# Kernel optimization log

Hardware: AMD Instinct MI355X
Metric: run time of the kernel (lower is better)

The kernel has to match this reference:

```python
import jax, jax.numpy as jnp
import numpy as np

INPUT_SIZE = 1024
HIDDEN_SIZE = 1024
BATCH = 8192
MLP_H1, MLP_H2 = 16, 8


def _uniform(key, shape, stdv):
    return jax.random.uniform(key, shape, jnp.float32, -stdv, stdv)


def setup_inputs() -> dict:
    key = jax.random.key(0)
    ks = jax.random.split(key, 20)
    stdv = 1.0 / np.sqrt(HIDDEN_SIZE)
    I, H = INPUT_SIZE, HIDDEN_SIZE
    inp = {
        "x": jax.random.normal(ks[0], (BATCH, I), jnp.float32),
        "h": jax.random.normal(ks[1], (BATCH, H), jnp.float32),
        "c": jax.random.normal(ks[2], (BATCH, H), jnp.float32),
        # gate weights (torch layout: matmul(h, W_h*) + matmul(x, W_x*) + b)
        "W_hi": _uniform(ks[3], (H, H), stdv),
        "W_xi": _uniform(ks[4], (I, H), stdv),
        "b_i": _uniform(ks[5], (H,), stdv),
        "W_hc": _uniform(ks[6], (H, H), stdv),
        "W_xc": _uniform(ks[7], (I, H), stdv),
        "b_c": _uniform(ks[8], (H,), stdv),
        "W_ho": _uniform(ks[9], (H, H), stdv),
        "W_xo": _uniform(ks[10], (I, H), stdv),
        "b_o": _uniform(ks[11], (H,), stdv),
        # forget MLP: (I+H) -> 16 -> 8 -> H, ReLU hidden, sigmoid output
        "W1": _uniform(ks[12], (I + H, MLP_H1), stdv),
        "b1": _uniform(ks[13], (MLP_H1,), stdv),
        "W2": _uniform(ks[14], (MLP_H1, MLP_H2), stdv),
        "b2": _uniform(ks[15], (MLP_H2,), stdv),
        "W3": _uniform(ks[16], (MLP_H2, H), stdv),
        "b3": _uniform(ks[17], (H,), stdv),
    }
    return inp


def reference(x, h, c, W_hi, W_xi, b_i, W_hc, W_xc, b_c, W_ho, W_xo, b_o,
              W1, b1, W2, b2, W3, b3):
    # forget gate via small MLP on concat(x, h)
    xh = jnp.concatenate((x, h), axis=1)           # [B, I+H]
    z = jax.nn.relu(xh @ W1 + b1)                  # [B, 16]
    z = jax.nn.relu(z @ W2 + b2)                   # [B, 8]
    f = jax.nn.sigmoid(z @ W3 + b3)                # [B, H]

    i = jax.nn.sigmoid(h @ W_hi + x @ W_xi + b_i)
    g = jnp.tanh(h @ W_hc + x @ W_xc + b_c)
    o = jax.nn.sigmoid(h @ W_ho + x @ W_xo + b_o)

    c_new = f * c + i * g
    h_new = o * jnp.tanh(c_new)
    return (h_new, c_new, f)
```

## Files before the change

### kernel.cpp

```cpp
#include <hip/hip_runtime.h>
#include <math.h>

#define BATCH 8192
#define HDIM  1024
#define KDIM  2048
#define NDIM  3072

typedef __attribute__((ext_vector_type(8))) short short8;
typedef __attribute__((ext_vector_type(4))) float floatx4;

__device__ __forceinline__ float b2f(unsigned short u) {
  union { unsigned int i; float f; } v; v.i = ((unsigned int)u) << 16; return v.f;
}
__device__ __forceinline__ unsigned short f2b(float f) {
  union { unsigned int i; float f; } v; v.f = f;
  unsigned int r = v.i + 0x7FFFu + ((v.i >> 16) & 1u);
  return (unsigned short)(r >> 16);
}
__device__ __forceinline__ float ldsel(const void* p, size_t i, int isbf) {
  return isbf ? b2f(((const unsigned short*)p)[i]) : ((const float*)p)[i];
}
__device__ __forceinline__ float sigf(float x) { return 1.0f / (1.0f + __expf(-x)); }
__device__ __forceinline__ float tanhfast(float x) {
  float a = __builtin_fabsf(x);
  float t = __expf(-2.f * a);
  float r = (1.f - t) / (1.f + t);
  return copysignf(r, x);
}

__device__ __forceinline__ int detect_bf(const void* x) {
  unsigned int w = ((const unsigned int*)x)[threadIdx.x & 63];
  unsigned short lo = (unsigned short)(w & 0xFFFFu);
  int e = (lo >> 7) & 0xFF;
  bool ok = (e >= 110 && e <= 135) || ((lo & 0x7FFFu) == 0);
  unsigned long long m = __ballot(ok);
  return (__popcll(m) >= 48) ? 1 : 0;
}

__device__ __forceinline__ void gld16(const void* g, void* l) {
  auto gp = reinterpret_cast<__attribute__((address_space(1))) unsigned int*>(
      (unsigned long long)g);
  auto lp = reinterpret_cast<__attribute__((address_space(3))) unsigned int*>(
      (unsigned long long)l);
  __builtin_amdgcn_global_load_lds(gp, lp, 16, 0, 0);
}

__device__ __forceinline__ short8 ld8bf(const void* p, size_t off, int isbf) {
  short8 r;
  if (isbf) {
    r = *(const short8*)((const unsigned short*)p + off);
  } else {
    const float* s = (const float*)p + off;
    float4 a = *(const float4*)(s);
    float4 b = *(const float4*)(s + 4);
    r[0]=(short)f2b(a.x); r[1]=(short)f2b(a.y); r[2]=(short)f2b(a.z); r[3]=(short)f2b(a.w);
    r[4]=(short)f2b(b.x); r[5]=(short)f2b(b.y); r[6]=(short)f2b(b.z); r[7]=(short)f2b(b.w);
  }
  return r;
}

__global__ __launch_bounds__(256) void k_z2(
    const void* __restrict__ x, const void* __restrict__ h,
    const void* __restrict__ W1, const void* __restrict__ b1,
    const void* __restrict__ W2, const void* __restrict__ b2,
    float* __restrict__ z2) {
  __shared__ __align__(16) char smem[70976];
  const int isbf = detect_bf(x);
  const int tid = threadIdx.x;
  unsigned short* lW = (unsigned short*)smem;
  float* part = (float*)(smem + 65536);
  float* z1s  = (float*)(smem + 69888);
  const int m0 = blockIdx.x * 16;
#pragma unroll
  for (int it = 0; it < 16; ++it) {
    const int chunk = it * 256 + tid;
    const int k = chunk >> 1;
    const int jh = (chunk & 1) * 8;
    unsigned short v[8];
    if (isbf) {
      short8 s = *(const short8*)((const unsigned short*)W1 + (size_t)k * 16 + jh);
#pragma unroll
      for (int j = 0; j < 8; ++j) v[j] = (unsigned short)s[j];
    } else {
      const float* s = (const float*)W1 + (size_t)k * 16 + jh;
      float4 a = *(const float4*)(s);
      float4 b = *(const float4*)(s + 4);
      v[0]=f2b(a.x); v[1]=f2b(a.y); v[2]=f2b(a.z); v[3]=f2b(a.w);
      v[4]=f2b(b.x); v[5]=f2b(b.y); v[6]=f2b(b.z); v[7]=f2b(b.w);
    }
#pragma unroll
    for (int j = 0; j < 8; ++j) {
      const int row = jh + j;
      lW[row * 2048 + (((k >> 3) ^ (row & 7)) << 3) + (k & 7)] = v[j];
    }
  }
  __syncthreads();
  const int w = tid >> 6;
  const int lane = tid & 63;
  const int q = lane >> 4;
  const int r = lane & 15;
  const void* src = (w >> 1) ? h : x;
  const size_t abase = (size_t)(m0 + r) * 1024 + (w & 1) * 512;
  const int kb = (w >> 1) * 1024 + (w & 1) * 512;
  floatx4 acc = {0.f, 0.f, 0.f, 0.f};
#pragma unroll 4
  for (int kt = 0; kt < 16; ++kt) {
    const int kl = kt * 32 + q * 8;
    short8 a = ld8bf(src, abase + kl, isbf);
    const int kg = kb + kl;
    short8 b = *(const short8*)(lW + r * 2048 + (((kg >> 3) ^ (r & 7)) << 3));
    acc = __builtin_amdgcn_mfma_f32_16x16x32_bf16(a, b, acc, 0, 0, 0);
  }
#pragma unroll
  for (int t = 0; t < 4; ++t) part[(w * 16 + q * 4 + t) * 17 + r] = acc[t];
  __syncthreads();
  {
    const int row = tid >> 4;
    const int n = tid & 15;
    float s = part[(0 * 16 + row) * 17 + n] + part[(1 * 16 + row) * 17 + n] +
              part[(2 * 16 + row) * 17 + n] + part[(3 * 16 + row) * 17 + n] +
              ldsel(b1, (size_t)n, isbf);
    z1s[row * 17 + n] = fmaxf(s, 0.f);
  }
  __syncthreads();
  if (tid < 128) {
    const int row = tid >> 3;
    const int p = tid & 7;
    float s = ldsel(b2, (size_t)p, isbf);
#pragma unroll
    for (int nn = 0; nn < 16; ++nn)
      s += z1s[row * 17 + nn] * ldsel(W2, (size_t)nn * 8 + p, isbf);
    z2[(size_t)(m0 + row) * 8 + p] = fmaxf(s, 0.f);
  }
}

__global__ __launch_bounds__(256) void k_wt(
    const void* __restrict__ x,
    const void* __restrict__ wxi, const void* __restrict__ whi,
    const void* __restrict__ wxc, const void* __restrict__ whc,
    const void* __restrict__ wxo, const void* __restrict__ who,
    unsigned short* __restrict__ WT) {
  __shared__ __align__(16) float tbuf[64][65];
  const int isbf = detect_bf(x);
  const int tid = threadIdx.x;
  const int b = blockIdx.x;
  const int mat = b >> 8;
  const int rem = b & 255;
  const int ti = rem >> 4;
  const int tj = rem & 15;
  const void* Ws[6] = {wxi, whi, wxc, whc, wxo, who};
  const void* W = Ws[mat];
  const int gt = mat >> 1;
  const int half = mat & 1;
  const int rrow = tid >> 3;
  const int c8 = (tid & 7) * 8;
#pragma unroll
  for (int it = 0; it < 2; ++it) {
    int row = it * 32 + rrow;
    size_t off = (size_t)(ti * 64 + row) * 1024 + tj * 64 + c8;
    if (isbf) {
      const unsigned short* s = (const unsigned short*)W + off;
      ushort4 a = *(const ushort4*)(s);
      ushort4 bv = *(const ushort4*)(s + 4);
      tbuf[row][c8+0]=b2f(a.x);  tbuf[row][c8+1]=b2f(a.y);
      tbuf[row][c8+2]=b2f(a.z);  tbuf[row][c8+3]=b2f(a.w);
      tbuf[row][c8+4]=b2f(bv.x); tbuf[row][c8+5]=b2f(bv.y);
      tbuf[row][c8+6]=b2f(bv.z); tbuf[row][c8+7]=b2f(bv.w);
    } else {
      const float* s = (const float*)W + off;
      float4 a = *(const float4*)(s);
      float4 bv = *(const float4*)(s + 4);
      tbuf[row][c8+0]=a.x;  tbuf[row][c8+1]=a.y;  tbuf[row][c8+2]=a.z;  tbuf[row][c8+3]=a.w;
      tbuf[row][c8+4]=bv.x; tbuf[row][c8+5]=bv.y; tbuf[row][c8+6]=bv.z; tbuf[row][c8+7]=bv.w;
    }
  }
  __syncthreads();
#pragma unroll
  for (int it = 0; it < 2; ++it) {
    int nl = it * 32 + rrow;
    int n = gt * 1024 + tj * 64 + nl;
    int kk = half * 1024 + ti * 64 + c8;
    short8 pk;
#pragma unroll
    for (int i = 0; i < 8; ++i) pk[i] = (short)f2b(tbuf[c8 + i][nl]);
    *(short8*)(WT + (size_t)n * KDIM + kk) = pk;
  }
}

__global__ __launch_bounds__(256) void k_apack(
    const void* __restrict__ x, const void* __restrict__ h,
    unsigned short* __restrict__ A) {
  if (detect_bf(x)) return;
  const size_t t0 = (size_t)blockIdx.x * 256 + threadIdx.x;
#pragma unroll
  for (int it = 0; it < 4; ++it) {
    const size_t idx = (t0 + (size_t)it * 524288) * 8;
    const int k = (int)(idx & 2047);
    const size_t m = idx >> 11;
    const float* s = (k < 1024) ? (const float*)x + m * 1024 + k
                                : (const float*)h + m * 1024 + (k - 1024);
    float4 a = *(const float4*)(s);
    float4 b = *(const float4*)(s + 4);
    short8 pk;
    pk[0]=(short)f2b(a.x); pk[1]=(short)f2b(a.y); pk[2]=(short)f2b(a.z); pk[3]=(short)f2b(a.w);
    pk[4]=(short)f2b(b.x); pk[5]=(short)f2b(b.y); pk[6]=(short)f2b(b.z); pk[7]=(short)f2b(b.w);
    *(short8*)(A + idx) = pk;
  }
}

__global__ __launch_bounds__(256, 3) void k_gemm(
    const void* __restrict__ x, const void* __restrict__ h,
    const unsigned short* __restrict__ Apack,
    const unsigned short* __restrict__ WT,
    unsigned short* __restrict__ P) {
  const int isbf = detect_bf(x);
  const unsigned short* Ax = isbf ? (const unsigned short*)x : Apack;
  const unsigned short* Ah = isbf ? (const unsigned short*)h : (Apack + 1024);
  const int sA = isbf ? 1024 : 2048;
  __shared__ __align__(16) unsigned short lA[128 * 64];
  __shared__ __align__(16) unsigned short lB[128 * 64];
  const int tid = threadIdx.x;
  const int lane = tid & 63;
  const int wv = tid >> 6;
  const int wm = (wv >> 1) << 6;
  const int wn = (wv & 1) << 6;
  const int m0 = blockIdx.y << 7;
  const int n0 = blockIdx.x << 7;

  floatx4 acc[4][4];
  const floatx4 fzero = {0.f, 0.f, 0.f, 0.f};
#pragma unroll
  for (int i = 0; i < 4; ++i)
#pragma unroll
    for (int j = 0; j < 4; ++j) acc[i][j] = fzero;

  int rr[4], kk[4];
#pragma unroll
  for (int ps = 0; ps < 4; ++ps) {
    int chunk = ps * 256 + tid;
    rr[ps] = chunk >> 3;
    kk[ps] = (chunk & 7) ^ (rr[ps] & 7);
  }
  const int px0 = (lane >> 4) ^ (lane & 7);
  const int px1 = ((lane >> 4) + 4) ^ (lane & 7);
  const int rowA = wm + (lane & 15);
  const int rowB = wn + (lane & 15);

  for (int kt = 0; kt < KDIM / 64; ++kt) {
    const int k0 = kt * 64;
    const unsigned short* Abase = (k0 < 1024) ? (Ax + k0) : (Ah + (k0 - 1024));
#pragma unroll
    for (int ps = 0; ps < 4; ++ps) {
      const int chunk = ps * 256 + tid;
      gld16(Abase + (size_t)(m0 + rr[ps]) * sA + kk[ps] * 8, lA + chunk * 8);
      gld16(WT + ((size_t)(n0 + rr[ps]) * KDIM + k0 + kk[ps] * 8), lB + chunk * 8);
    }
    __syncthreads();
#pragma unroll
    for (int s = 0; s < 2; ++s) {
      const int px = s ? px1 : px0;
      short8 af[4], bfr[4];
#pragma unroll
      for (int i = 0; i < 4; ++i)
        af[i] = *(const short8*)(lA + ((((rowA + (i << 4)) << 3) + px) << 3));
#pragma unroll
      for (int i = 0; i < 4; ++i)
        bfr[i] = *(const short8*)(lB + ((((rowB + (i << 4)) << 3) + px) << 3));
#pragma unroll
      for (int mi = 0; mi < 4; ++mi)
#pragma unroll
        for (int ni = 0; ni < 4; ++ni)
          acc[mi][ni] = __builtin_amdgcn_mfma_f32_16x16x32_bf16(
              af[mi], bfr[ni], acc[mi][ni], 0, 0, 0);
    }
    __syncthreads();
  }
  const int col = lane & 15;
  const int rq = (lane >> 4) << 2;
#pragma unroll
  for (int mi = 0; mi < 4; ++mi) {
#pragma unroll
    for (int ni = 0; ni < 4; ++ni) {
      const size_t n = (size_t)(n0 + wn + (ni << 4) + col);
#pragma unroll
      for (int t = 0; t < 4; ++t) {
        const size_t m = (size_t)(m0 + wm + (mi << 4) + rq + t);
        P[m * NDIM + n] = f2b(acc[mi][ni][t]);
      }
    }
  }
}

__global__ __launch_bounds__(256) void k_pointwise(
    const unsigned short* __restrict__ P, const void* __restrict__ x,
    const void* __restrict__ cin,
    const void* __restrict__ bi, const void* __restrict__ bc,
    const void* __restrict__ bo, const float* __restrict__ z2,
    const void* __restrict__ W3, const void* __restrict__ b3,
    void* __restrict__ out) {
  const int isbf = detect_bf(x);
  const int tid = threadIdx.x;
  const int n = tid * 4;
  const size_t MH = (size_t)BATCH * HDIM;

  float w3r[8][4], bif[4], bcf[4], bof[4], b3f[4];
  if (isbf) {
#pragma unroll
    for (int j = 0; j < 8; ++j) {
      ushort4 u = *(const ushort4*)((const unsigned short*)W3 + j * 1024 + n);
      w3r[j][0]=b2f(u.x); w3r[j][1]=b2f(u.y); w3r[j][2]=b2f(u.z); w3r[j][3]=b2f(u.w);
    }
    ushort4 u3 = *(const ushort4*)((const unsigned short*)b3 + n);
    b3f[0]=b2f(u3.x); b3f[1]=b2f(u3.y); b3f[2]=b2f(u3.z); b3f[3]=b2f(u3.w);
    ushort4 a = *(const ushort4*)((const unsigned short*)bi + n);
    ushort4 b = *(const ushort4*)((const unsigned short*)bc + n);
    ushort4 d = *(const ushort4*)((const unsigned short*)bo + n);
    bif[0]=b2f(a.x); bif[1]=b2f(a.y); bif[2]=b2f(a.z); bif[3]=b2f(a.w);
    bcf[0]=b2f(b.x); bcf[1]=b2f(b.y); bcf[2]=b2f(b.z); bcf[3]=b2f(b.w);
    bof[0]=b2f(d.x); bof[1]=b2f(d.y); bof[2]=b2f(d.z); bof[3]=b2f(d.w);
  } else {
#pragma unroll
    for (int j = 0; j < 8; ++j) {
      float4 u = *(const float4*)((const float*)W3 + j * 1024 + n);
      w3r[j][0]=u.x; w3r[j][1]=u.y; w3r[j][2]=u.z; w3r[j][3]=u.w;
    }
    float4 u3 = *(const float4*)((const float*)b3 + n);
    b3f[0]=u3.x; b3f[1]=u3.y; b3f[2]=u3.z; b3f[3]=u3.w;
    float4 a = *(const float4*)((const float*)bi + n);
    float4 b = *(const float4*)((const float*)bc + n);
    float4 d = *(const float4*)((const float*)bo + n);
    bif[0]=a.x; bif[1]=a.y; bif[2]=a.z; bif[3]=a.w;
    bcf[0]=b.x; bcf[1]=b.y; bcf[2]=b.z; bcf[3]=b.w;
    bof[0]=d.x; bof[1]=d.y; bof[2]=d.z; bof[3]=d.w;
  }

  const size_t m0 = (size_t)blockIdx.x * 8;
#pragma unroll
  for (int rI = 0; rI < 8; ++rI) {
    const size_t m = m0 + rI;
    const size_t idx = m * 1024 + n;
    const unsigned short* pr = P + m * NDIM + n;
    ushort4 ui = *(const ushort4*)(pr);
    ushort4 ug = *(const ushort4*)(pr + 1024);
    ushort4 uo = *(const ushort4*)(pr + 2048);
    float pi[4] = {b2f(ui.x), b2f(ui.y), b2f(ui.z), b2f(ui.w)};
    float pg[4] = {b2f(ug.x), b2f(ug.y), b2f(ug.z), b2f(ug.w)};
    float po[4] = {b2f(uo.x), b2f(uo.y), b2f(uo.z), b2f(uo.w)};
    float4 za = *(const float4*)(z2 + m * 8);
    float4 zb = *(const float4*)(z2 + m * 8 + 4);
    float zz[8] = {za.x, za.y, za.z, za.w, zb.x, zb.y, zb.z, zb.w};
    float cf[4];
    if (isbf) {
      ushort4 e = *(const ushort4*)((const unsigned short*)cin + idx);
      cf[0]=b2f(e.x); cf[1]=b2f(e.y); cf[2]=b2f(e.z); cf[3]=b2f(e.w);
    } else {
      float4 e = *(const float4*)((const float*)cin + idx);
      cf[0]=e.x; cf[1]=e.y; cf[2]=e.z; cf[3]=e.w;
    }
    float f3[4] = {b3f[0], b3f[1], b3f[2], b3f[3]};
#pragma unroll
    for (int j = 0; j < 8; ++j) {
      f3[0] += zz[j] * w3r[j][0];
      f3[1] += zz[j] * w3r[j][1];
      f3[2] += zz[j] * w3r[j][2];
      f3[3] += zz[j] * w3r[j][3];
    }
    float hn[4], cn[4], ff[4];
#pragma unroll
    for (int t = 0; t < 4; ++t) {
      float F = sigf(f3[t]);
      float I = sigf(pi[t] + bif[t]);
      float G = tanhfast(pg[t] + bcf[t]);
      float O = sigf(po[t] + bof[t]);
      float C = F * cf[t] + I * G;
      ff[t] = F;
      cn[t] = C;
      hn[t] = O * tanhfast(C);
    }
    if (isbf) {
      unsigned short* ob = (unsigned short*)out;
      *(ushort4*)(ob + idx) = make_ushort4(f2b(hn[0]), f2b(hn[1]), f2b(hn[2]), f2b(hn[3]));
      *(ushort4*)(ob + MH + idx) = make_ushort4(f2b(cn[0]), f2b(cn[1]), f2b(cn[2]), f2b(cn[3]));
      *(ushort4*)(ob + 2 * MH + idx) = make_ushort4(f2b(ff[0]), f2b(ff[1]), f2b(ff[2]), f2b(ff[3]));
    } else {
      float* ob = (float*)out;
      *(float4*)(ob + idx) = make_float4(hn[0], hn[1], hn[2], hn[3]);
      *(float4*)(ob + MH + idx) = make_float4(cn[0], cn[1], cn[2], cn[3]);
      *(float4*)(ob + 2 * MH + idx) = make_float4(ff[0], ff[1], ff[2], ff[3]);
    }
  }
}

extern "C" void kernel_launch(void* const* d_in, const int* in_sizes, int n_in,
                              void* d_out, int out_size, void* d_ws, size_t ws_size,
                              hipStream_t stream) {
  const void* x    = d_in[0];
  const void* h    = d_in[1];
  const void* c    = d_in[2];
  const void* W_hi = d_in[3];
  const void* W_xi = d_in[4];
  const void* b_i  = d_in[5];
  const void* W_hc = d_in[6];
  const void* W_xc = d_in[7];
  const void* b_c  = d_in[8];
  const void* W_ho = d_in[9];
  const void* W_xo = d_in[10];
  const void* b_o  = d_in[11];
  const void* W1   = d_in[12];
  const void* b1   = d_in[13];
  const void* W2   = d_in[14];
  const void* b2   = d_in[15];
  const void* W3   = d_in[16];
  const void* b3   = d_in[17];

  char* ws = (char*)d_ws;
  unsigned short* A   = (unsigned short*)ws;
  unsigned short* WT  = (unsigned short*)(ws + 33554432);
  unsigned short* P   = (unsigned short*)(ws + 46137344);
  float*          z2b = (float*)(ws + 96468992);

  k_apack<<<dim3(2048), dim3(256), 0, stream>>>(x, h, A);
  k_wt<<<dim3(1536), dim3(256), 0, stream>>>(x, W_xi, W_hi, W_xc, W_hc,
                                             W_xo, W_ho, WT);
  k_z2<<<dim3(512), dim3(256), 0, stream>>>(x, h, W1, b1, W2, b2, z2b);
  k_gemm<<<dim3(NDIM / 128, BATCH / 128), dim3(256), 0, stream>>>(x, h, A, WT, P);
  k_pointwise<<<dim3(BATCH / 8), dim3(256), 0, stream>>>(P, x, c, b_i, b_c, b_o,
                                                         z2b, W3, b3, d_out);
}
```

Before: 364.9 us.

## Fuse gate GEMM with LSTM pointwise epilogue and fold A packing into MLP kernel

The k_apack kernel goes away, and the k_z2 kernel now writes the bf16-packed x|h matrix as a side effect of reading it for the forget MLP. The GEMM is restructured so each block computes a 128x64 tile for all three gates at once, with three accumulator groups. The full LSTM pointwise math runs in the GEMM epilogue, which removes the intermediate P buffer round trip and the separate pointwise kernel. A grouped block-index swizzle is added for L2 reuse. The cost is higher register pressure (96 accumulators per thread, and occupancy hint dropped), plus epilogue stores that are scalar and strided rather than vectorized.

```diff
diff --git a/kernel.cpp b/kernel.cpp
--- a/kernel.cpp
+++ b/kernel.cpp
@@ -4,7 +4,6 @@
 #define BATCH 8192
 #define HDIM  1024
 #define KDIM  2048
-#define NDIM  3072
 
 typedef __attribute__((ext_vector_type(8))) short short8;
 typedef __attribute__((ext_vector_type(4))) float floatx4;
@@ -63,7 +62,7 @@
     const void* __restrict__ x, const void* __restrict__ h,
     const void* __restrict__ W1, const void* __restrict__ b1,
     const void* __restrict__ W2, const void* __restrict__ b2,
-    float* __restrict__ z2) {
+    unsigned short* __restrict__ A, float* __restrict__ z2) {
   __shared__ __align__(16) char smem[70976];
   const int isbf = detect_bf(x);
   const int tid = threadIdx.x;
@@ -108,6 +107,7 @@
     const int kl = kt * 32 + q * 8;
     short8 a = ld8bf(src, abase + kl, isbf);
     const int kg = kb + kl;
+    if (!isbf) *(short8*)(A + (size_t)(m0 + r) * KDIM + kg) = a;
     short8 b = *(const short8*)(lW + r * 2048 + (((kg >> 3) ^ (r & 7)) << 3));
     acc = __builtin_amdgcn_mfma_f32_16x16x32_bf16(a, b, acc, 0, 0, 0);
   }
@@ -187,59 +187,58 @@
   }
 }
 
-__global__ __launch_bounds__(256) void k_apack(
-    const void* __restrict__ x, const void* __restrict__ h,
-    unsigned short* __restrict__ A) {
-  if (detect_bf(x)) return;
-  const size_t t0 = (size_t)blockIdx.x * 256 + threadIdx.x;
-#pragma unroll
-  for (int it = 0; it < 4; ++it) {
-    const size_t idx = (t0 + (size_t)it * 524288) * 8;
-    const int k = (int)(idx & 2047);
-    const size_t m = idx >> 11;
-    const float* s = (k < 1024) ? (const float*)x + m * 1024 + k
-                                : (const float*)h + m * 1024 + (k - 1024);
-    float4 a = *(const float4*)(s);
-    float4 b = *(const float4*)(s + 4);
-    short8 pk;
-    pk[0]=(short)f2b(a.x); pk[1]=(short)f2b(a.y); pk[2]=(short)f2b(a.z); pk[3]=(short)f2b(a.w);
-    pk[4]=(short)f2b(b.x); pk[5]=(short)f2b(b.y); pk[6]=(short)f2b(b.z); pk[7]=(short)f2b(b.w);
-    *(short8*)(A + idx) = pk;
-  }
-}
-
-__global__ __launch_bounds__(256, 3) void k_gemm(
+__global__ __launch_bounds__(256) void k_gemm_f(
     const void* __restrict__ x, const void* __restrict__ h,
     const unsigned short* __restrict__ Apack,
     const unsigned short* __restrict__ WT,
-    unsigned short* __restrict__ P) {
+    const void* __restrict__ cin,
+    const void* __restrict__ bi, const void* __restrict__ bc,
+    const void* __restrict__ bo,
+    const float* __restrict__ z2,
+    const void* __restrict__ W3, const void* __restrict__ b3,
+    void* __restrict__ out) {
   const int isbf = detect_bf(x);
   const unsigned short* Ax = isbf ? (const unsigned short*)x : Apack;
   const unsigned short* Ah = isbf ? (const unsigned short*)h : (Apack + 1024);
-  const int sA = isbf ? 1024 : 2048;
-  __shared__ __align__(16) unsigned short lA[128 * 64];
-  __shared__ __align__(16) unsigned short lB[128 * 64];
+  const int sA = isbf ? 1024 : KDIM;
+  __shared__ __align__(16) char smem[40960];
+  unsigned short* lA = (unsigned short*)smem;
+  unsigned short* lB = (unsigned short*)(smem + 16384);
   const int tid = threadIdx.x;
   const int lane = tid & 63;
   const int wv = tid >> 6;
   const int wm = (wv >> 1) << 6;
-  const int wn = (wv & 1) << 6;
-  const int m0 = blockIdx.y << 7;
-  const int n0 = blockIdx.x << 7;
-
-  floatx4 acc[4][4];
+  const int wn = (wv & 1) << 5;
+
+  const int bid = blockIdx.x;
+  const int swz = ((bid & 7) << 7) | (bid >> 3);
+  const int m0 = (swz >> 4) << 7;
+  const int n0 = (swz & 15) << 6;
+
+  floatx4 acc[3][4][2];
   const floatx4 fzero = {0.f, 0.f, 0.f, 0.f};
 #pragma unroll
-  for (int i = 0; i < 4; ++i)
-#pragma unroll
-    for (int j = 0; j < 4; ++j) acc[i][j] = fzero;
-
-  int rr[4], kk[4];
+  for (int g = 0; g < 3; ++g)
+#pragma unroll
+    for (int i = 0; i < 4; ++i)
+#pragma unroll
+      for (int j = 0; j < 2; ++j) acc[g][i][j] = fzero;
+
+  int rrA[4], kkA[4];
 #pragma unroll
   for (int ps = 0; ps < 4; ++ps) {
-    int chunk = ps * 256 + tid;
-    rr[ps] = chunk >> 3;
-    kk[ps] = (chunk & 7) ^ (rr[ps] & 7);
+    int c = ps * 256 + tid;
+    rrA[ps] = c >> 3;
+    kkA[ps] = (c & 7) ^ (rrA[ps] & 7);
+  }
+  int gB[6], rrB[6], kkB[6];
+#pragma unroll
+  for (int ps = 0; ps < 6; ++ps) {
+    int c = ps * 256 + tid;
+    gB[ps] = c >> 9;
+    int cl = c & 511;
+    rrB[ps] = cl >> 3;
+    kkB[ps] = (cl & 7) ^ (rrB[ps] & 7);
   }
   const int px0 = (lane >> 4) ^ (lane & 7);
   const int px1 = ((lane >> 4) + 4) ^ (lane & 7);
@@ -251,142 +250,95 @@
     const unsigned short* Abase = (k0 < 1024) ? (Ax + k0) : (Ah + (k0 - 1024));
 #pragma unroll
     for (int ps = 0; ps < 4; ++ps) {
-      const int chunk = ps * 256 + tid;
-      gld16(Abase + (size_t)(m0 + rr[ps]) * sA + kk[ps] * 8, lA + chunk * 8);
-      gld16(WT + ((size_t)(n0 + rr[ps]) * KDIM + k0 + kk[ps] * 8), lB + chunk * 8);
+      const int c = ps * 256 + tid;
+      gld16(Abase + (size_t)(m0 + rrA[ps]) * sA + kkA[ps] * 8, lA + c * 8);
+    }
+#pragma unroll
+    for (int ps = 0; ps < 6; ++ps) {
+      const int c = ps * 256 + tid;
+      gld16(WT + ((size_t)(gB[ps] * 1024 + n0 + rrB[ps]) * KDIM + k0 + kkB[ps] * 8),
+            lB + c * 8);
     }
     __syncthreads();
 #pragma unroll
     for (int s = 0; s < 2; ++s) {
       const int px = s ? px1 : px0;
-      short8 af[4], bfr[4];
+      short8 af[4], bfr[3][2];
 #pragma unroll
       for (int i = 0; i < 4; ++i)
         af[i] = *(const short8*)(lA + ((((rowA + (i << 4)) << 3) + px) << 3));
 #pragma unroll
-      for (int i = 0; i < 4; ++i)
-        bfr[i] = *(const short8*)(lB + ((((rowB + (i << 4)) << 3) + px) << 3));
-#pragma unroll
-      for (int mi = 0; mi < 4; ++mi)
-#pragma unroll
-        for (int ni = 0; ni < 4; ++ni)
-          acc[mi][ni] = __builtin_amdgcn_mfma_f32_16x16x32_bf16(
-              af[mi], bfr[ni], acc[mi][ni], 0, 0, 0);
+      for (int g = 0; g < 3; ++g)
+#pragma unroll
+        for (int j = 0; j < 2; ++j)
+          bfr[g][j] = *(const short8*)(lB + (g << 12) +
+                                       ((((rowB + (j << 4)) << 3) + px) << 3));
+#pragma unroll
+      for (int g = 0; g < 3; ++g)
+#pragma unroll
+        for (int mi = 0; mi < 4; ++mi)
+#pragma unroll
+          for (int ni = 0; ni < 2; ++ni)
+            acc[g][mi][ni] = __builtin_amdgcn_mfma_f32_16x16x32_bf16(
+                af[mi], bfr[g][ni], acc[g][mi][ni], 0, 0, 0);
     }
     __syncthreads();
   }
-  const int col = lane & 15;
+
+  float* z2s = (float*)smem;
+  *(float4*)(z2s + tid * 4) = *(const float4*)(z2 + (size_t)m0 * 8 + tid * 4);
+  __syncthreads();
+
+  const int col_l = lane & 15;
   const int rq = (lane >> 4) << 2;
+  float w3c[2][8], b3c[2], bic[2], bcc[2], boc[2];
+#pragma unroll
+  for (int ni = 0; ni < 2; ++ni) {
+    const size_t n_g = (size_t)(n0 + wn + (ni << 4) + col_l);
+    b3c[ni] = ldsel(b3, n_g, isbf);
+    bic[ni] = ldsel(bi, n_g, isbf);
+    bcc[ni] = ldsel(bc, n_g, isbf);
+    boc[ni] = ldsel(bo, n_g, isbf);
+#pragma unroll
+    for (int j = 0; j < 8; ++j) w3c[ni][j] = ldsel(W3, (size_t)j * 1024 + n_g, isbf);
+  }
+  const size_t MH = (size_t)BATCH * HDIM;
 #pragma unroll
   for (int mi = 0; mi < 4; ++mi) {
 #pragma unroll
-    for (int ni = 0; ni < 4; ++ni) {
-      const size_t n = (size_t)(n0 + wn + (ni << 4) + col);
-#pragma unroll
-      for (int t = 0; t < 4; ++t) {
-        const size_t m = (size_t)(m0 + wm + (mi << 4) + rq + t);
-        P[m * NDIM + n] = f2b(acc[mi][ni][t]);
+    for (int t = 0; t < 4; ++t) {
+      const int rloc = wm + (mi << 4) + rq + t;
+      const size_t m_g = (size_t)m0 + rloc;
+      float zz[8];
+#pragma unroll
+      for (int j = 0; j < 8; ++j) zz[j] = z2s[rloc * 8 + j];
+#pragma unroll
+      for (int ni = 0; ni < 2; ++ni) {
+        const size_t n_g = (size_t)(n0 + wn + (ni << 4) + col_l);
+        const size_t idx = m_g * HDIM + n_g;
+        float f3 = b3c[ni];
+#pragma unroll
+        for (int j = 0; j < 8; ++j) f3 += zz[j] * w3c[ni][j];
+        const float cf = isbf ? b2f(((const unsigned short*)cin)[idx])
+                              : ((const float*)cin)[idx];
+        const float F = sigf(f3);
+        const float I = sigf(acc[0][mi][ni][t] + bic[ni]);
+        const float G = tanhfast(acc[1][mi][ni][t] + bcc[ni]);
+        const float O = sigf(acc[2][mi][ni][t] + boc[ni]);
+        const float C = F * cf + I * G;
+        const float HN = O * tanhfast(C);
+        if (isbf) {
+          unsigned short* ob = (unsigned short*)out;
+          ob[idx] = f2b(HN);
+          ob[MH + idx] = f2b(C);
+          ob[2 * MH + idx] = f2b(F);
+        } else {
+          float* ob = (float*)out;
+          ob[idx] = HN;
+          ob[MH + idx] = C;
+          ob[2 * MH + idx] = F;
+        }
       }
-    }
-  }
-}
-
-__global__ __launch_bounds__(256) void k_pointwise(
-    const unsigned short* __restrict__ P, const void* __restrict__ x,
-    const void* __restrict__ cin,
-    const void* __restrict__ bi, const void* __restrict__ bc,
-    const void* __restrict__ bo, const float* __restrict__ z2,
-    const void* __restrict__ W3, const void* __restrict__ b3,
-    void* __restrict__ out) {
-  const int isbf = detect_bf(x);
-  const int tid = threadIdx.x;
-  const int n = tid * 4;
-  const size_t MH = (size_t)BATCH * HDIM;
-
-  float w3r[8][4], bif[4], bcf[4], bof[4], b3f[4];
-  if (isbf) {
-#pragma unroll
-    for (int j = 0; j < 8; ++j) {
-      ushort4 u = *(const ushort4*)((const unsigned short*)W3 + j * 1024 + n);
-      w3r[j][0]=b2f(u.x); w3r[j][1]=b2f(u.y); w3r[j][2]=b2f(u.z); w3r[j][3]=b2f(u.w);
-    }
-    ushort4 u3 = *(const ushort4*)((const unsigned short*)b3 + n);
-    b3f[0]=b2f(u3.x); b3f[1]=b2f(u3.y); b3f[2]=b2f(u3.z); b3f[3]=b2f(u3.w);
-    ushort4 a = *(const ushort4*)((const unsigned short*)bi + n);
-    ushort4 b = *(const ushort4*)((const unsigned short*)bc + n);
-    ushort4 d = *(const ushort4*)((const unsigned short*)bo + n);
-    bif[0]=b2f(a.x); bif[1]=b2f(a.y); bif[2]=b2f(a.z); bif[3]=b2f(a.w);
-    bcf[0]=b2f(b.x); bcf[1]=b2f(b.y); bcf[2]=b2f(b.z); bcf[3]=b2f(b.w);
-    bof[0]=b2f(d.x); bof[1]=b2f(d.y); bof[2]=b2f(d.z); bof[3]=b2f(d.w);
-  } else {
-#pragma unroll
-    for (int j = 0; j < 8; ++j) {
-      float4 u = *(const float4*)((const float*)W3 + j * 1024 + n);
-      w3r[j][0]=u.x; w3r[j][1]=u.y; w3r[j][2]=u.z; w3r[j][3]=u.w;
-    }
-    float4 u3 = *(const float4*)((const float*)b3 + n);
-    b3f[0]=u3.x; b3f[1]=u3.y; b3f[2]=u3.z; b3f[3]=u3.w;
-    float4 a = *(const float4*)((const float*)bi + n);
-    float4 b = *(const float4*)((const float*)bc + n);
-    float4 d = *(const float4*)((const float*)bo + n);
-    bif[0]=a.x; bif[1]=a.y; bif[2]=a.z; bif[3]=a.w;
-    bcf[0]=b.x; bcf[1]=b.y; bcf[2]=b.z; bcf[3]=b.w;
-    bof[0]=d.x; bof[1]=d.y; bof[2]=d.z; bof[3]=d.w;
-  }
-
-  const size_t m0 = (size_t)blockIdx.x * 8;
-#pragma unroll
-  for (int rI = 0; rI < 8; ++rI) {
-    const size_t m = m0 + rI;
-    const size_t idx = m * 1024 + n;
-    const unsigned short* pr = P + m * NDIM + n;
-    ushort4 ui = *(const ushort4*)(pr);
-    ushort4 ug = *(const ushort4*)(pr + 1024);
-    ushort4 uo = *(const ushort4*)(pr + 2048);
-    float pi[4] = {b2f(ui.x), b2f(ui.y), b2f(ui.z), b2f(ui.w)};
-    float pg[4] = {b2f(ug.x), b2f(ug.y), b2f(ug.z), b2f(ug.w)};
-    float po[4] = {b2f(uo.x), b2f(uo.y), b2f(uo.z), b2f(uo.w)};
-    float4 za = *(const float4*)(z2 + m * 8);
-    float4 zb = *(const float4*)(z2 + m * 8 + 4);
-    float zz[8] = {za.x, za.y, za.z, za.w, zb.x, zb.y, zb.z, zb.w};
-    float cf[4];
-    if (isbf) {
-      ushort4 e = *(const ushort4*)((const unsigned short*)cin + idx);
-      cf[0]=b2f(e.x); cf[1]=b2f(e.y); cf[2]=b2f(e.z); cf[3]=b2f(e.w);
-    } else {
-      float4 e = *(const float4*)((const float*)cin + idx);
-      cf[0]=e.x; cf[1]=e.y; cf[2]=e.z; cf[3]=e.w;
-    }
-    float f3[4] = {b3f[0], b3f[1], b3f[2], b3f[3]};
-#pragma unroll
-    for (int j = 0; j < 8; ++j) {
-      f3[0] += zz[j] * w3r[j][0];
-      f3[1] += zz[j] * w3r[j][1];
-      f3[2] += zz[j] * w3r[j][2];
-      f3[3] += zz[j] * w3r[j][3];
-    }
-    float hn[4], cn[4], ff[4];
-#pragma unroll
-    for (int t = 0; t < 4; ++t) {
-      float F = sigf(f3[t]);
-      float I = sigf(pi[t] + bif[t]);
-      float G = tanhfast(pg[t] + bcf[t]);
-      float O = sigf(po[t] + bof[t]);
-      float C = F * cf[t] + I * G;
-      ff[t] = F;
-      cn[t] = C;
-      hn[t] = O * tanhfast(C);
-    }
-    if (isbf) {
-      unsigned short* ob = (unsigned short*)out;
-      *(ushort4*)(ob + idx) = make_ushort4(f2b(hn[0]), f2b(hn[1]), f2b(hn[2]), f2b(hn[3]));
-      *(ushort4*)(ob + MH + idx) = make_ushort4(f2b(cn[0]), f2b(cn[1]), f2b(cn[2]), f2b(cn[3]));
-      *(ushort4*)(ob + 2 * MH + idx) = make_ushort4(f2b(ff[0]), f2b(ff[1]), f2b(ff[2]), f2b(ff[3]));
-    } else {
-      float* ob = (float*)out;
-      *(float4*)(ob + idx) = make_float4(hn[0], hn[1], hn[2], hn[3]);
-      *(float4*)(ob + MH + idx) = make_float4(cn[0], cn[1], cn[2], cn[3]);
-      *(float4*)(ob + 2 * MH + idx) = make_float4(ff[0], ff[1], ff[2], ff[3]);
     }
   }
 }
@@ -416,14 +368,11 @@
   char* ws = (char*)d_ws;
   unsigned short* A   = (unsigned short*)ws;
   unsigned short* WT  = (unsigned short*)(ws + 33554432);
-  unsigned short* P   = (unsigned short*)(ws + 46137344);
   float*          z2b = (float*)(ws + 96468992);
 
-  k_apack<<<dim3(2048), dim3(256), 0, stream>>>(x, h, A);
+  k_z2<<<dim3(512), dim3(256), 0, stream>>>(x, h, W1, b1, W2, b2, A, z2b);
   k_wt<<<dim3(1536), dim3(256), 0, stream>>>(x, W_xi, W_hi, W_xc, W_hc,
                                              W_xo, W_ho, WT);
-  k_z2<<<dim3(512), dim3(256), 0, stream>>>(x, h, W1, b1, W2, b2, z2b);
-  k_gemm<<<dim3(NDIM / 128, BATCH / 128), dim3(256), 0, stream>>>(x, h, A, WT, P);
-  k_pointwise<<<dim3(BATCH / 8), dim3(256), 0, stream>>>(P, x, c, b_i, b_c, b_o,
-                                                         z2b, W3, b3, d_out);
-}
+  k_gemm_f<<<dim3(1024), dim3(256), 0, stream>>>(x, h, A, WT, c, b_i, b_c, b_o,
+                                                 z2b, W3, b3, d_out);
+}
```

Result: slower. 375.6 us (+2.9%).

## Fuse bf16 packing of x/h into the forget-MLP first-layer kernel

Applied to the files above, without the earlier changes.

Merges the separate activation packing kernel (fp32 x,h to bf16 A) into the kernel computing the forget MLP's first two layers. The activations are now read once and used both to write the packed A buffer and to feed the small MFMA. W1 is streamed per k-tile through shared memory instead of being staged whole, which cuts LDS use. This saves one launch and one full read of x and h, but adds a sync per k-tile and gives a smaller grid for the packing work.

```diff
diff --git a/kernel.cpp b/kernel.cpp
--- a/kernel.cpp
+++ b/kernel.cpp
@@ -59,57 +59,79 @@
   return r;
 }
 
-__global__ __launch_bounds__(256) void k_z2(
+__global__ __launch_bounds__(256) void k_prep(
     const void* __restrict__ x, const void* __restrict__ h,
     const void* __restrict__ W1, const void* __restrict__ b1,
     const void* __restrict__ W2, const void* __restrict__ b2,
-    float* __restrict__ z2) {
-  __shared__ __align__(16) char smem[70976];
+    unsigned short* __restrict__ A, float* __restrict__ z2) {
+  __shared__ __align__(16) unsigned short tA[16 * 256];
+  __shared__ __align__(16) unsigned short tB[16 * 256];
+  __shared__ float part[4 * 16 * 17];
+  __shared__ float z1s[16 * 17];
   const int isbf = detect_bf(x);
   const int tid = threadIdx.x;
-  unsigned short* lW = (unsigned short*)smem;
-  float* part = (float*)(smem + 65536);
-  float* z1s  = (float*)(smem + 69888);
   const int m0 = blockIdx.x * 16;
-#pragma unroll
-  for (int it = 0; it < 16; ++it) {
-    const int chunk = it * 256 + tid;
-    const int k = chunk >> 1;
-    const int jh = (chunk & 1) * 8;
-    unsigned short v[8];
-    if (isbf) {
-      short8 s = *(const short8*)((const unsigned short*)W1 + (size_t)k * 16 + jh);
-#pragma unroll
-      for (int j = 0; j < 8; ++j) v[j] = (unsigned short)s[j];
-    } else {
-      const float* s = (const float*)W1 + (size_t)k * 16 + jh;
-      float4 a = *(const float4*)(s);
-      float4 b = *(const float4*)(s + 4);
-      v[0]=f2b(a.x); v[1]=f2b(a.y); v[2]=f2b(a.z); v[3]=f2b(a.w);
-      v[4]=f2b(b.x); v[5]=f2b(b.y); v[6]=f2b(b.z); v[7]=f2b(b.w);
-    }
-#pragma unroll
-    for (int j = 0; j < 8; ++j) {
-      const int row = jh + j;
-      lW[row * 2048 + (((k >> 3) ^ (row & 7)) << 3) + (k & 7)] = v[j];
-    }
-  }
-  __syncthreads();
+  const int lane = tid & 63;
   const int w = tid >> 6;
-  const int lane = tid & 63;
   const int q = lane >> 4;
   const int r = lane & 15;
-  const void* src = (w >> 1) ? h : x;
-  const size_t abase = (size_t)(m0 + r) * 1024 + (w & 1) * 512;
-  const int kb = (w >> 1) * 1024 + (w & 1) * 512;
+  char* tAb = (char*)tA;
+  char* tBb = (char*)tB;
+
+  const int arow = tid >> 4;
+  const int ak = (tid & 15) * 16;
+
   floatx4 acc = {0.f, 0.f, 0.f, 0.f};
-#pragma unroll 4
-  for (int kt = 0; kt < 16; ++kt) {
-    const int kl = kt * 32 + q * 8;
-    short8 a = ld8bf(src, abase + kl, isbf);
-    const int kg = kb + kl;
-    short8 b = *(const short8*)(lW + r * 2048 + (((kg >> 3) ^ (r & 7)) << 3));
-    acc = __builtin_amdgcn_mfma_f32_16x16x32_bf16(a, b, acc, 0, 0, 0);
+
+  for (int ktile = 0; ktile < 8; ++ktile) {
+    const int k0 = ktile * 256;
+    const void* src = (k0 < 1024) ? x : h;
+    const int klocal = (k0 & 1023) + ak;
+    short8 v0 = ld8bf(src, (size_t)(m0 + arow) * 1024 + klocal, isbf);
+    short8 v1 = ld8bf(src, (size_t)(m0 + arow) * 1024 + klocal + 8, isbf);
+    float wv[16];
+    if (isbf) {
+      const unsigned short* s = (const unsigned short*)W1 + (size_t)(k0 + tid) * 16;
+      short8 s0 = *(const short8*)(s);
+      short8 s1 = *(const short8*)(s + 8);
+#pragma unroll
+      for (int j = 0; j < 8; ++j) { wv[j] = b2f((unsigned short)s0[j]);
+                                    wv[8 + j] = b2f((unsigned short)s1[j]); }
+    } else {
+      const float* s = (const float*)W1 + (size_t)(k0 + tid) * 16;
+      float4 a0 = *(const float4*)(s);
+      float4 a1 = *(const float4*)(s + 4);
+      float4 a2 = *(const float4*)(s + 8);
+      float4 a3 = *(const float4*)(s + 12);
+      wv[0]=a0.x; wv[1]=a0.y; wv[2]=a0.z; wv[3]=a0.w;
+      wv[4]=a1.x; wv[5]=a1.y; wv[6]=a1.z; wv[7]=a1.w;
+      wv[8]=a2.x; wv[9]=a2.y; wv[10]=a2.z; wv[11]=a2.w;
+      wv[12]=a3.x; wv[13]=a3.y; wv[14]=a3.z; wv[15]=a3.w;
+    }
+    if (!isbf) {
+      unsigned short* Ao = A + (size_t)(m0 + arow) * KDIM + k0 + ak;
+      *(short8*)(Ao) = v0;
+      *(short8*)(Ao + 8) = v1;
+    }
+    {
+      const int base = arow * 512 + ak * 2;
+      const int sw = (arow & 7) << 4;
+      *(short8*)(tAb + ((base) ^ sw)) = v0;
+      *(short8*)(tAb + ((base + 16) ^ sw)) = v1;
+    }
+#pragma unroll
+    for (int j = 0; j < 16; ++j) {
+      *(unsigned short*)(tBb + ((j * 512 + tid * 2) ^ ((j & 7) << 4))) = f2b(wv[j]);
+    }
+    __syncthreads();
+#pragma unroll
+    for (int s = 0; s < 2; ++s) {
+      const int ks = (w * 2 + s) * 32 + q * 8;
+      short8 af = *(const short8*)(tAb + ((r * 512 + ks * 2) ^ ((r & 7) << 4)));
+      short8 bf = *(const short8*)(tBb + ((r * 512 + ks * 2) ^ ((r & 7) << 4)));
+      acc = __builtin_amdgcn_mfma_f32_16x16x32_bf16(af, bf, acc, 0, 0, 0);
+    }
+    __syncthreads();
   }
 #pragma unroll
   for (int t = 0; t < 4; ++t) part[(w * 16 + q * 4 + t) * 17 + r] = acc[t];
@@ -184,27 +206,6 @@
 #pragma unroll
     for (int i = 0; i < 8; ++i) pk[i] = (short)f2b(tbuf[c8 + i][nl]);
     *(short8*)(WT + (size_t)n * KDIM + kk) = pk;
-  }
-}
-
-__global__ __launch_bounds__(256) void k_apack(
-    const void* __restrict__ x, const void* __restrict__ h,
-    unsigned short* __restrict__ A) {
-  if (detect_bf(x)) return;
-  const size_t t0 = (size_t)blockIdx.x * 256 + threadIdx.x;
-#pragma unroll
-  for (int it = 0; it < 4; ++it) {
-    const size_t idx = (t0 + (size_t)it * 524288) * 8;
-    const int k = (int)(idx & 2047);
-    const size_t m = idx >> 11;
-    const float* s = (k < 1024) ? (const float*)x + m * 1024 + k
-                                : (const float*)h + m * 1024 + (k - 1024);
-    float4 a = *(const float4*)(s);
-    float4 b = *(const float4*)(s + 4);
-    short8 pk;
-    pk[0]=(short)f2b(a.x); pk[1]=(short)f2b(a.y); pk[2]=(short)f2b(a.z); pk[3]=(short)f2b(a.w);
-    pk[4]=(short)f2b(b.x); pk[5]=(short)f2b(b.y); pk[6]=(short)f2b(b.z); pk[7]=(short)f2b(b.w);
-    *(short8*)(A + idx) = pk;
   }
 }
 
@@ -419,10 +420,9 @@
   unsigned short* P   = (unsigned short*)(ws + 46137344);
   float*          z2b = (float*)(ws + 96468992);
 
-  k_apack<<<dim3(2048), dim3(256), 0, stream>>>(x, h, A);
+  k_prep<<<dim3(512), dim3(256), 0, stream>>>(x, h, W1, b1, W2, b2, A, z2b);
   k_wt<<<dim3(1536), dim3(256), 0, stream>>>(x, W_xi, W_hi, W_xc, W_hc,
                                              W_xo, W_ho, WT);
-  k_z2<<<dim3(512), dim3(256), 0, stream>>>(x, h, W1, b1, W2, b2, z2b);
   k_gemm<<<dim3(NDIM / 128, BATCH / 128), dim3(256), 0, stream>>>(x, h, A, WT, P);
   k_pointwise<<<dim3(BATCH / 8), dim3(256), 0, stream>>>(P, x, c, b_i, b_c, b_o,
                                                          z2b, W3, b3, d_out);
```

New measurement: 351.2 us. 3.8% less time.
